# Optimization experiments

Hardware: AMD Instinct MI355X
Metric: run time of the kernel (lower is better)

The kernel has to match this reference:

```python
import jax, jax.numpy as jnp
import numpy as np

# uniform-size batching: B graphs, NC compound atoms, NP pocket residues each
B, NC, NP, H = 16, 64, 384, 128
CFEAT, PFEAT = 56, 1280
SCALE = 5.0  # coordinate_scale
LN_EPS = 1e-5


def setup_inputs() -> dict:
    key = jax.random.key(0)
    ks = jax.random.split(key, 16)
    inp = {
        "compound_feats": jax.random.normal(ks[0], (B * NC, CFEAT), jnp.float32),
        "pocket_feats": jax.random.normal(ks[1], (B * NP, PFEAT), jnp.float32),
        "complex_coords": jax.random.normal(ks[2], (B, 2 + NC + NP, 3), jnp.float32) * 10.0,
        "pocket_xyz": jax.random.normal(ks[3], (B, NP, 3), jnp.float32) * 10.0,
        "dis_map": jax.random.uniform(ks[4], (B * NP * NC,), jnp.float32) * 10.0,
        # learned parameters (xavier with gain=0.001 as in the torch init)
        "Wc": jax.random.normal(ks[5], (CFEAT, H), jnp.float32) * 0.001,
        "bc": jnp.zeros((H,), jnp.float32),
        "Wp": jax.random.normal(ks[6], (PFEAT, H), jnp.float32) * 0.001,
        "bp": jnp.zeros((H,), jnp.float32),
        "ln_g": jnp.ones((H,), jnp.float32),
        "ln_b": jnp.zeros((H,), jnp.float32),
        "W1": jax.random.normal(ks[7], (H, H), jnp.float32) * 0.001,
        "b1": jnp.zeros((H,), jnp.float32),
        "W2": jax.random.normal(ks[8], (H, 1), jnp.float32) * 0.001,
        "b2": jnp.zeros((1,), jnp.float32),
    }
    return inp


def _layernorm(x, g, b):
    m = jnp.mean(x, axis=-1, keepdims=True)
    v = jnp.mean(jnp.square(x - m), axis=-1, keepdims=True)
    return (x - m) * jax.lax.rsqrt(v + LN_EPS) * g + b


def reference(compound_feats, pocket_feats, complex_coords, pocket_xyz, dis_map,
              Wc, bc, Wp, bp, ln_g, ln_b, W1, b1, W2, b2):
    norm = lambda x: x / SCALE
    # input linears, then dense-batch (uniform sizes -> exact reshape)
    comp_emb = (compound_feats @ Wc + bc).reshape(B, NC, H)   # [B,NC,H]
    pock_emb = (pocket_feats @ Wp + bp).reshape(B, NP, H)     # [B,NP,H]
    # complex layout per graph: [glb_c, compound (NC), glb_p, pocket (NP)]
    # complex_binding_model treated as identity (see notes): emb/coords pass through.
    comp_coords_out = norm(complex_coords[:, 1:1 + NC])       # [B,NC,3] (normalized)
    pock_coords = norm(pocket_xyz)                            # [B,NP,3]
    # torch.cdist(pocket, compound): [B,NP,NC]
    diff = pock_coords[:, :, None, :] - comp_coords_out[:, None, :, :]
    pc_dis = jnp.sqrt(jnp.sum(jnp.square(diff), axis=-1))
    # layernorm + pairwise outer product + distmap MLP
    p_ln = _layernorm(pock_emb, ln_g, ln_b)
    c_ln = _layernorm(comp_emb, ln_g, ln_b)
    z = jnp.einsum('bik,bjk->bijk', p_ln, c_ln)               # [B,NP,NC,H]
    h = jax.nn.relu(z @ W1 + b1)
    b_logit = (h @ W2 + b2)[..., 0]                            # [B,NP,NC]
    # uniform sizes -> all-true masks, boolean-select is a flatten
    dis_map_pred_by_pair = jax.nn.sigmoid(b_logit.reshape(-1)) * 10.0
    dis_map_pred_by_coord = jnp.clip(pc_dis.reshape(-1) * SCALE, 0.0, 10.0)
    compound_coord_pred = (comp_coords_out * SCALE).reshape(B * NC, 3)
    compound_batch = jnp.repeat(jnp.arange(B, dtype=jnp.int32), NC)
    return (compound_coord_pred, compound_batch, dis_map_pred_by_pair,
            dis_map_pred_by_coord, dis_map)
```

## Files before the change

### kernel.cpp

```cpp
#include <hip/hip_runtime.h>
#include <hip/hip_bf16.h>

#define BB 16
#define NC 64
#define NP 384
#define HH 128
#define CF 56
#define PFT 1280

typedef float f32x4 __attribute__((ext_vector_type(4)));
typedef __bf16 bf16x8 __attribute__((ext_vector_type(8)));
typedef unsigned short u16x8 __attribute__((ext_vector_type(8)));
typedef unsigned short u16x4 __attribute__((ext_vector_type(4)));

static __device__ __forceinline__ unsigned short f2bfu(float f){
  __bf16 h = (__bf16)f;
  return __builtin_bit_cast(unsigned short, h);
}
static __device__ __forceinline__ float bfu2f(unsigned short u){
  __bf16 h = __builtin_bit_cast(__bf16, u);
  return (float)h;
}

__global__ __launch_bounds__(256) void k_prep(
    const float* __restrict__ cf, const float* __restrict__ Wc,
    const float* __restrict__ bc, const float* __restrict__ lng,
    const float* __restrict__ lnb, const float* __restrict__ Wp,
    const float* __restrict__ W1, const float* __restrict__ cc,
    const float* __restrict__ px, const float* __restrict__ dm,
    unsigned short* __restrict__ c_ln, unsigned short* __restrict__ wpt,
    unsigned short* __restrict__ w1t,
    float* __restrict__ out1, float* __restrict__ out4, float* __restrict__ out5){
  __shared__ unsigned short t[128][72];
  __shared__ float redc[2][2], redc2[2][2];
  int bx = blockIdx.x;
  int tid = threadIdx.x;
  if (bx < 20){
    int k0 = bx*64;
    #pragma unroll
    for (int i=0;i<8;i++){
      int fi = tid + i*256;
      int k  = fi>>5;
      int c4 = (fi&31)*4;
      float4 v = *(const float4*)(Wp + (size_t)(k0+k)*HH + c4);
      t[c4+0][k]=f2bfu(v.x); t[c4+1][k]=f2bfu(v.y);
      t[c4+2][k]=f2bfu(v.z); t[c4+3][k]=f2bfu(v.w);
    }
    __syncthreads();
    #pragma unroll
    for (int i=0;i<4;i++){
      int ci = tid + i*256;
      int col = ci>>3, kb = ci&7;
      u16x8 v = *(const u16x8*)&t[col][kb*8];
      *(u16x8*)(wpt + (size_t)col*PFT + k0 + kb*8) = v;
    }
  } else if (bx < 84){
    int idx = (bx-20)*256+tid;
    int k = idx>>7, m = idx&127;
    w1t[m*HH+k] = f2bfu(W1[idx]);
  } else if (bx < 596){
    int rh = tid>>7, m = tid&127;
    int row = (bx-84)*2 + rh;
    const float* cr = cf + row*CF;
    float acc = bc[m];
    #pragma unroll
    for (int k=0;k<CF;k++) acc += cr[k]*Wc[k*HH+m];
    float s=acc, s2=acc*acc;
    #pragma unroll
    for (int off=1; off<64; off<<=1){ s += __shfl_xor(s,off,64); s2 += __shfl_xor(s2,off,64); }
    int wid = (tid>>6)&1;
    if ((m&63)==0){ redc[rh][wid]=s; redc2[rh][wid]=s2; }
    __syncthreads();
    float S=redc[rh][0]+redc[rh][1], S2=redc2[rh][0]+redc2[rh][1];
    float mean = S*(1.0f/HH);
    float var  = S2*(1.0f/HH) - mean*mean;
    float rs = rsqrtf(var + 1e-5f);
    c_ln[(size_t)row*HH+m] = f2bfu((acc-mean)*rs*lng[m] + lnb[m]);
  } else if (bx < 608){
    int idx = (bx-596)*256+tid;
    if (idx < BB*NC*3){
      int bb = idx/(NC*3), rem = idx%(NC*3);
      float v = cc[(size_t)bb*(2+NC+NP)*3 + 3 + rem];
      out1[idx] = (v/5.0f)*5.0f;
    }
    if (idx < BB*NC) out1[BB*NC*3+idx] = (float)(idx>>6);
  } else {
    int idx = (bx-608)*256+tid;
    int b = idx/(NP*NC), r = idx%(NP*NC), i = r>>6, j = r&63;
    const float* pp = px + ((size_t)b*NP+i)*3;
    const float* cp = cc + (size_t)b*(2+NC+NP)*3 + 3 + (size_t)j*3;
    float dx=pp[0]/5.0f-cp[0]/5.0f;
    float dy=pp[1]/5.0f-cp[1]/5.0f;
    float dz=pp[2]/5.0f-cp[2]/5.0f;
    float d = sqrtf(dx*dx+dy*dy+dz*dz)*5.0f;
    d = fminf(fmaxf(d,0.f),10.f);
    out4[idx]=d;
    out5[idx]=dm[idx];
  }
}

__global__ __launch_bounds__(256,2) void k_main(
    const float* __restrict__ pf, const unsigned short* __restrict__ wpt,
    const float* __restrict__ bp, const float* __restrict__ lng,
    const float* __restrict__ lnb,
    const unsigned short* __restrict__ c_ln, const unsigned short* __restrict__ w1t,
    const float* __restrict__ b1, const float* __restrict__ W2,
    const float* __restrict__ b2p, float* __restrict__ out3){
  __shared__ __align__(16) unsigned short sA[2][16*64];
  __shared__ __align__(16) unsigned short sB[2][HH*64];
  __shared__ __align__(16) float sPf[12*HH];
  int tid = threadIdx.x;
  int w = tid>>6, lane = tid&63, q = lane&15, gr = lane>>4;
  int bx = blockIdx.x;
  int b  = bx>>5;
  int i0 = (bx&31)*12;
  size_t prow0 = (size_t)(b*NP + i0);
  *(unsigned short*)((char*)&sA[0][0] + 1536 + tid*2) = 0;
  *(unsigned short*)((char*)&sA[1][0] + 1536 + tid*2) = 0;
  f32x4 acc2[2];
  acc2[0]=(f32x4){0.f,0.f,0.f,0.f}; acc2[1]=(f32x4){0.f,0.f,0.f,0.f};
  int arow = tid>>4, ak4 = (tid&15)*4;
  float4 ra; u16x8 rb[4];
  #define LOADS1(KS) {                                                         \
    int kbase = (KS)*64;                                                       \
    if (arow < 12)                                                             \
      ra = *(const float4*)(pf + (prow0+arow)*PFT + kbase + ak4);              \
    _Pragma("unroll")                                                          \
    for (int i=0;i<4;i++){                                                     \
      int bi = tid + 256*i;                                                    \
      int col = bi>>3, kb = bi&7;                                              \
      rb[i] = *(const u16x8*)(wpt + (size_t)col*PFT + kbase + kb*8);           \
    }                                                                          \
  }
  #define WRITES1(BUF) {                                                       \
    char* A = (char*)&sA[BUF][0];                                              \
    char* Bc = (char*)&sB[BUF][0];                                             \
    if (arow < 12){                                                            \
      u16x4 h = { f2bfu(ra.x), f2bfu(ra.y), f2bfu(ra.z), f2bfu(ra.w) };        \
      *(u16x4*)(A + arow*128 + (((ak4>>3)^(arow&7))<<4) + ((ak4&7)<<1)) = h;   \
    }                                                                          \
    _Pragma("unroll")                                                          \
    for (int i=0;i<4;i++){                                                     \
      int bi = tid + 256*i;                                                    \
      int col = bi>>3, kb = bi&7;                                              \
      *(u16x8*)(Bc + col*128 + ((kb^(col&7))<<4)) = rb[i];                     \
    }                                                                          \
  }
  LOADS1(0)
  WRITES1(0)
  int cur = 0;
  for (int ks=0; ks<20; ks++){
    if (ks<19) LOADS1(ks+1)
    __syncthreads();
    char* A = (char*)&sA[cur][0];
    char* Bc = (char*)&sB[cur][0];
    #pragma unroll
    for (int kk=0;kk<2;kk++){
      bf16x8 a = *(bf16x8*)(A + q*128 + (((kk*4+gr)^(q&7))<<4));
      #pragma unroll
      for (int ct=0;ct<2;ct++){
        int col = w*32 + ct*16 + q;
        bf16x8 bfr = *(bf16x8*)(Bc + col*128 + (((kk*4+gr)^(col&7))<<4));
        acc2[ct] = __builtin_amdgcn_mfma_f32_16x16x32_bf16(a,bfr,acc2[ct],0,0,0);
      }
    }
    if (ks<19){ WRITES1(cur^1) cur ^= 1; }
  }
  __syncthreads();
  #pragma unroll
  for (int ct=0;ct<2;ct++){
    int col = w*32 + ct*16 + q;
    float bpv = bp[col];
    #pragma unroll
    for (int r=0;r<4;r++){
      int row = gr*4+r;
      if (row < 12) sPf[row*HH + col] = acc2[ct][r] + bpv;
    }
  }
  float cfr[4][8];
  {
    const unsigned short* cb = c_ln + (size_t)b*NC*HH + (size_t)(w*16+q)*HH + gr*8;
    #pragma unroll
    for (int kt=0;kt<4;kt++){
      u16x8 v = *(const u16x8*)(cb + kt*32);
      #pragma unroll
      for (int e=0;e<8;e++) cfr[kt][e] = bfu2f(v[e]);
    }
  }
  bf16x8 w1f[4][8];
  #pragma unroll
  for (int kt=0;kt<4;kt++)
    #pragma unroll
    for (int nt=0;nt<8;nt++)
      w1f[kt][nt] = *(const bf16x8*)(w1t + (size_t)(nt*16+q)*HH + kt*32 + gr*8);
  float b1v[8], w2v[8];
  #pragma unroll
  for (int nt=0;nt<8;nt++){ b1v[nt]=b1[nt*16+q]; w2v[nt]=W2[nt*16+q]; }
  float b2 = b2p[0];
  __syncthreads();
  {
    float g0 = lng[lane], g1 = lng[lane+64];
    float B0 = lnb[lane], B1 = lnb[lane+64];
    #pragma unroll
    for (int rr=0; rr<3; rr++){
      int row = w*3+rr;
      float a0 = sPf[row*HH + lane], a1 = sPf[row*HH + lane + 64];
      float s = a0+a1, s2 = a0*a0 + a1*a1;
      #pragma unroll
      for (int off=1; off<64; off<<=1){ s += __shfl_xor(s,off,64); s2 += __shfl_xor(s2,off,64); }
      float mean = s*(1.0f/HH);
      float var  = s2*(1.0f/HH) - mean*mean;
      float rs   = rsqrtf(var + 1e-5f);
      sPf[row*HH + lane]      = (a0-mean)*rs*g0 + B0;
      sPf[row*HH + lane + 64] = (a1-mean)*rs*g1 + B1;
    }
  }
  __syncthreads();
  for (int ii=0; ii<12; ii++){
    f32x4 acc[8];
    #pragma unroll
    for (int nt=0;nt<8;nt++) acc[nt]=(f32x4){0.f,0.f,0.f,0.f};
    #pragma unroll
    for (int kt=0;kt<4;kt++){
      f32x4 p0 = *(const f32x4*)&sPf[ii*HH + kt*32 + gr*8];
      f32x4 p1 = *(const f32x4*)&sPf[ii*HH + kt*32 + gr*8 + 4];
      bf16x8 a;
      #pragma unroll
      for (int e=0;e<4;e++) a[e]   = (__bf16)(cfr[kt][e]*p0[e]);
      #pragma unroll
      for (int e=0;e<4;e++) a[e+4] = (__bf16)(cfr[kt][e+4]*p1[e]);
      #pragma unroll
      for (int nt=0;nt<8;nt++)
        acc[nt] = __builtin_amdgcn_mfma_f32_16x16x32_bf16(a, w1f[kt][nt], acc[nt], 0,0,0);
    }
    float part[4]={0.f,0.f,0.f,0.f};
    #pragma unroll
    for (int nt=0;nt<8;nt++)
      #pragma unroll
      for (int r=0;r<4;r++){
        float h = acc[nt][r] + b1v[nt];
        h = fmaxf(h, 0.f);
        part[r] += h*w2v[nt];
      }
    #pragma unroll
    for (int r=0;r<4;r++){
      part[r]+=__shfl_xor(part[r],1,16);
      part[r]+=__shfl_xor(part[r],2,16);
      part[r]+=__shfl_xor(part[r],4,16);
      part[r]+=__shfl_xor(part[r],8,16);
    }
    if (q==0){
      float4 o;
      o.x = 10.f/(1.f+expf(-(part[0]+b2)));
      o.y = 10.f/(1.f+expf(-(part[1]+b2)));
      o.z = 10.f/(1.f+expf(-(part[2]+b2)));
      o.w = 10.f/(1.f+expf(-(part[3]+b2)));
      *(float4*)(out3 + (prow0+ii)*NC + w*16 + gr*4) = o;
    }
  }
}

extern "C" void kernel_launch(void* const* d_in, const int* in_sizes, int n_in,
                              void* d_out, int out_size, void* d_ws, size_t ws_size,
                              hipStream_t stream){
  const float* cf = (const float*)d_in[0];
  const float* pf = (const float*)d_in[1];
  const float* cc = (const float*)d_in[2];
  const float* px = (const float*)d_in[3];
  const float* dm = (const float*)d_in[4];
  const float* Wc = (const float*)d_in[5];
  const float* bc = (const float*)d_in[6];
  const float* Wp = (const float*)d_in[7];
  const float* bp = (const float*)d_in[8];
  const float* lng= (const float*)d_in[9];
  const float* lnb= (const float*)d_in[10];
  const float* W1 = (const float*)d_in[11];
  const float* b1 = (const float*)d_in[12];
  const float* W2 = (const float*)d_in[13];
  const float* b2 = (const float*)d_in[14];

  float* out = (float*)d_out;
  char* ws = (char*)d_ws;
  unsigned short* c_ln = (unsigned short*)ws;
  unsigned short* w1t  = (unsigned short*)(ws + 262144 + 1572864);
  unsigned short* wpt  = (unsigned short*)(ws + 262144 + 1572864 + 32768);

  float* out1 = out;
  float* out3 = out + BB*NC*3 + BB*NC;
  float* out4 = out3 + BB*NP*NC;
  float* out5 = out4 + BB*NP*NC;

  hipLaunchKernelGGL(k_prep, dim3(2144), dim3(256), 0, stream,
                     cf, Wc, bc, lng, lnb, Wp, W1, cc, px, dm,
                     c_ln, wpt, w1t, out1, out4, out5);
  hipLaunchKernelGGL(k_main, dim3(512), dim3(256), 0, stream,
                     pf, wpt, bp, lng, lnb, c_ln, w1t, b1, W2, b2, out3);
}
```

Measured before the change: 44.67 us.

## Load pocket GEMM operands directly to registers and use 32x32 MFMA for pair MLP

The pocket projection GEMM drops its LDS double-buffered staging. Each wave now loads A (fp32, converted to bf16) and B fragments straight from global memory into registers, with no barriers in the K loop. The pair MLP switches from 16x16x32 to 32x32x16 MFMA with a 2x2 wave split over compound atoms and hidden units. It processes two pocket rows per iteration and streams W1 fragments from global/L2, and partial logits are combined through shared memory before the sigmoid. This cuts LDS traffic and syncs and raises MFMA efficiency, at the cost of more uncoalesced global loads, a 32-wide shuffle reduction, and dropping the 2-blocks-per-SIMD occupancy hint.

```diff
diff --git a/kernel.cpp b/kernel.cpp
--- a/kernel.cpp
+++ b/kernel.cpp
@@ -9,9 +9,9 @@
 #define PFT 1280
 
 typedef float f32x4 __attribute__((ext_vector_type(4)));
+typedef float f32x16 __attribute__((ext_vector_type(16)));
 typedef __bf16 bf16x8 __attribute__((ext_vector_type(8)));
 typedef unsigned short u16x8 __attribute__((ext_vector_type(8)));
-typedef unsigned short u16x4 __attribute__((ext_vector_type(4)));
 
 static __device__ __forceinline__ unsigned short f2bfu(float f){
   __bf16 h = (__bf16)f;
@@ -99,103 +99,65 @@
   }
 }
 
-__global__ __launch_bounds__(256,2) void k_main(
+__global__ __launch_bounds__(256) void k_main(
     const float* __restrict__ pf, const unsigned short* __restrict__ wpt,
     const float* __restrict__ bp, const float* __restrict__ lng,
     const float* __restrict__ lnb,
     const unsigned short* __restrict__ c_ln, const unsigned short* __restrict__ w1t,
     const float* __restrict__ b1, const float* __restrict__ W2,
     const float* __restrict__ b2p, float* __restrict__ out3){
-  __shared__ __align__(16) unsigned short sA[2][16*64];
-  __shared__ __align__(16) unsigned short sB[2][HH*64];
   __shared__ __align__(16) float sPf[12*HH];
+  __shared__ __align__(16) float psumh[2][12][64];
   int tid = threadIdx.x;
   int w = tid>>6, lane = tid&63, q = lane&15, gr = lane>>4;
   int bx = blockIdx.x;
   int b  = bx>>5;
   int i0 = (bx&31)*12;
   size_t prow0 = (size_t)(b*NP + i0);
-  *(unsigned short*)((char*)&sA[0][0] + 1536 + tid*2) = 0;
-  *(unsigned short*)((char*)&sA[1][0] + 1536 + tid*2) = 0;
   f32x4 acc2[2];
   acc2[0]=(f32x4){0.f,0.f,0.f,0.f}; acc2[1]=(f32x4){0.f,0.f,0.f,0.f};
-  int arow = tid>>4, ak4 = (tid&15)*4;
-  float4 ra; u16x8 rb[4];
-  #define LOADS1(KS) {                                                         \
-    int kbase = (KS)*64;                                                       \
-    if (arow < 12)                                                             \
-      ra = *(const float4*)(pf + (prow0+arow)*PFT + kbase + ak4);              \
-    _Pragma("unroll")                                                          \
-    for (int i=0;i<4;i++){                                                     \
-      int bi = tid + 256*i;                                                    \
-      int col = bi>>3, kb = bi&7;                                              \
-      rb[i] = *(const u16x8*)(wpt + (size_t)col*PFT + kbase + kb*8);           \
-    }                                                                          \
-  }
-  #define WRITES1(BUF) {                                                       \
-    char* A = (char*)&sA[BUF][0];                                              \
-    char* Bc = (char*)&sB[BUF][0];                                             \
-    if (arow < 12){                                                            \
-      u16x4 h = { f2bfu(ra.x), f2bfu(ra.y), f2bfu(ra.z), f2bfu(ra.w) };        \
-      *(u16x4*)(A + arow*128 + (((ak4>>3)^(arow&7))<<4) + ((ak4&7)<<1)) = h;   \
-    }                                                                          \
-    _Pragma("unroll")                                                          \
-    for (int i=0;i<4;i++){                                                     \
-      int bi = tid + 256*i;                                                    \
-      int col = bi>>3, kb = bi&7;                                              \
-      *(u16x8*)(Bc + col*128 + ((kb^(col&7))<<4)) = rb[i];                     \
-    }                                                                          \
-  }
-  LOADS1(0)
-  WRITES1(0)
-  int cur = 0;
+  int arow = q<12 ? q : 11;
+  const float* pA = pf + (prow0+arow)*PFT;
+  const unsigned short* pB0 = wpt + (size_t)(w*32+q)*PFT;
+  const unsigned short* pB1 = wpt + (size_t)(w*32+16+q)*PFT;
+  #pragma unroll 4
   for (int ks=0; ks<20; ks++){
-    if (ks<19) LOADS1(ks+1)
-    __syncthreads();
-    char* A = (char*)&sA[cur][0];
-    char* Bc = (char*)&sB[cur][0];
-    #pragma unroll
-    for (int kk=0;kk<2;kk++){
-      bf16x8 a = *(bf16x8*)(A + q*128 + (((kk*4+gr)^(q&7))<<4));
-      #pragma unroll
-      for (int ct=0;ct<2;ct++){
-        int col = w*32 + ct*16 + q;
-        bf16x8 bfr = *(bf16x8*)(Bc + col*128 + (((kk*4+gr)^(col&7))<<4));
-        acc2[ct] = __builtin_amdgcn_mfma_f32_16x16x32_bf16(a,bfr,acc2[ct],0,0,0);
-      }
-    }
-    if (ks<19){ WRITES1(cur^1) cur ^= 1; }
-  }
-  __syncthreads();
-  #pragma unroll
-  for (int ct=0;ct<2;ct++){
-    int col = w*32 + ct*16 + q;
-    float bpv = bp[col];
+    #pragma unroll
+    for (int kk=0; kk<2; kk++){
+      int k0 = ks*64 + kk*32 + gr*8;
+      float4 a0 = *(const float4*)(pA + k0);
+      float4 a1 = *(const float4*)(pA + k0 + 4);
+      u16x8 ub0 = *(const u16x8*)(pB0 + k0);
+      u16x8 ub1 = *(const u16x8*)(pB1 + k0);
+      bf16x8 a;
+      a[0]=(__bf16)a0.x; a[1]=(__bf16)a0.y; a[2]=(__bf16)a0.z; a[3]=(__bf16)a0.w;
+      a[4]=(__bf16)a1.x; a[5]=(__bf16)a1.y; a[6]=(__bf16)a1.z; a[7]=(__bf16)a1.w;
+      acc2[0] = __builtin_amdgcn_mfma_f32_16x16x32_bf16(a, __builtin_bit_cast(bf16x8, ub0), acc2[0], 0,0,0);
+      acc2[1] = __builtin_amdgcn_mfma_f32_16x16x32_bf16(a, __builtin_bit_cast(bf16x8, ub1), acc2[1], 0,0,0);
+    }
+  }
+  {
+    float bp0 = bp[w*32+q], bp1 = bp[w*32+16+q];
     #pragma unroll
     for (int r=0;r<4;r++){
       int row = gr*4+r;
-      if (row < 12) sPf[row*HH + col] = acc2[ct][r] + bpv;
-    }
-  }
-  float cfr[4][8];
+      if (row<12){
+        sPf[row*HH + w*32+q]      = acc2[0][r] + bp0;
+        sPf[row*HH + w*32+16+q]   = acc2[1][r] + bp1;
+      }
+    }
+  }
+  int l31 = lane&31, gr2 = lane>>5;
+  int jh = w&1, mh = w>>1;
+  int j0 = jh*32, m0 = mh*64;
+  u16x8 cfrag[8];
   {
-    const unsigned short* cb = c_ln + (size_t)b*NC*HH + (size_t)(w*16+q)*HH + gr*8;
-    #pragma unroll
-    for (int kt=0;kt<4;kt++){
-      u16x8 v = *(const u16x8*)(cb + kt*32);
-      #pragma unroll
-      for (int e=0;e<8;e++) cfr[kt][e] = bfu2f(v[e]);
-    }
-  }
-  bf16x8 w1f[4][8];
-  #pragma unroll
-  for (int kt=0;kt<4;kt++)
-    #pragma unroll
-    for (int nt=0;nt<8;nt++)
-      w1f[kt][nt] = *(const bf16x8*)(w1t + (size_t)(nt*16+q)*HH + kt*32 + gr*8);
-  float b1v[8], w2v[8];
-  #pragma unroll
-  for (int nt=0;nt<8;nt++){ b1v[nt]=b1[nt*16+q]; w2v[nt]=W2[nt*16+q]; }
+    const unsigned short* cbase = c_ln + ((size_t)b*NC + j0 + l31)*HH + gr2*8;
+    #pragma unroll
+    for (int ksp=0;ksp<8;ksp++) cfrag[ksp] = *(const u16x8*)(cbase + ksp*16);
+  }
+  float b1v0=b1[m0+l31], b1v1=b1[m0+32+l31];
+  float w2v0=W2[m0+l31], w2v1=W2[m0+32+l31];
   float b2 = b2p[0];
   __syncthreads();
   {
@@ -216,47 +178,71 @@
     }
   }
   __syncthreads();
-  for (int ii=0; ii<12; ii++){
-    f32x4 acc[8];
-    #pragma unroll
-    for (int nt=0;nt<8;nt++) acc[nt]=(f32x4){0.f,0.f,0.f,0.f};
-    #pragma unroll
-    for (int kt=0;kt<4;kt++){
-      f32x4 p0 = *(const f32x4*)&sPf[ii*HH + kt*32 + gr*8];
-      f32x4 p1 = *(const f32x4*)&sPf[ii*HH + kt*32 + gr*8 + 4];
-      bf16x8 a;
-      #pragma unroll
-      for (int e=0;e<4;e++) a[e]   = (__bf16)(cfr[kt][e]*p0[e]);
-      #pragma unroll
-      for (int e=0;e<4;e++) a[e+4] = (__bf16)(cfr[kt][e+4]*p1[e]);
-      #pragma unroll
-      for (int nt=0;nt<8;nt++)
-        acc[nt] = __builtin_amdgcn_mfma_f32_16x16x32_bf16(a, w1f[kt][nt], acc[nt], 0,0,0);
-    }
-    float part[4]={0.f,0.f,0.f,0.f};
-    #pragma unroll
-    for (int nt=0;nt<8;nt++)
-      #pragma unroll
-      for (int r=0;r<4;r++){
-        float h = acc[nt][r] + b1v[nt];
-        h = fmaxf(h, 0.f);
-        part[r] += h*w2v[nt];
+  const unsigned short* wb0 = w1t + (size_t)(m0+l31)*HH + gr2*8;
+  const unsigned short* wb1 = w1t + (size_t)(m0+32+l31)*HH + gr2*8;
+  for (int ip=0; ip<6; ip++){
+    f32x16 accA0, accA1, accB0, accB1;
+    #pragma unroll
+    for (int r=0;r<16;r++){ accA0[r]=0.f; accA1[r]=0.f; accB0[r]=0.f; accB1[r]=0.f; }
+    int iiA = ip*2, iiB = ip*2+1;
+    #pragma unroll
+    for (int ksp=0; ksp<8; ksp++){
+      bf16x8 bv0 = __builtin_bit_cast(bf16x8, *(const u16x8*)(wb0 + ksp*16));
+      bf16x8 bv1 = __builtin_bit_cast(bf16x8, *(const u16x8*)(wb1 + ksp*16));
+      u16x8 cfv = cfrag[ksp];
+      {
+        f32x4 p0 = *(const f32x4*)&sPf[iiA*HH + ksp*16 + gr2*8];
+        f32x4 p1 = *(const f32x4*)&sPf[iiA*HH + ksp*16 + gr2*8 + 4];
+        bf16x8 a;
+        a[0]=(__bf16)(bfu2f(cfv[0])*p0[0]); a[1]=(__bf16)(bfu2f(cfv[1])*p0[1]);
+        a[2]=(__bf16)(bfu2f(cfv[2])*p0[2]); a[3]=(__bf16)(bfu2f(cfv[3])*p0[3]);
+        a[4]=(__bf16)(bfu2f(cfv[4])*p1[0]); a[5]=(__bf16)(bfu2f(cfv[5])*p1[1]);
+        a[6]=(__bf16)(bfu2f(cfv[6])*p1[2]); a[7]=(__bf16)(bfu2f(cfv[7])*p1[3]);
+        accA0 = __builtin_amdgcn_mfma_f32_32x32x16_bf16(a, bv0, accA0, 0,0,0);
+        accA1 = __builtin_amdgcn_mfma_f32_32x32x16_bf16(a, bv1, accA1, 0,0,0);
       }
-    #pragma unroll
-    for (int r=0;r<4;r++){
-      part[r]+=__shfl_xor(part[r],1,16);
-      part[r]+=__shfl_xor(part[r],2,16);
-      part[r]+=__shfl_xor(part[r],4,16);
-      part[r]+=__shfl_xor(part[r],8,16);
-    }
-    if (q==0){
-      float4 o;
-      o.x = 10.f/(1.f+expf(-(part[0]+b2)));
-      o.y = 10.f/(1.f+expf(-(part[1]+b2)));
-      o.z = 10.f/(1.f+expf(-(part[2]+b2)));
-      o.w = 10.f/(1.f+expf(-(part[3]+b2)));
-      *(float4*)(out3 + (prow0+ii)*NC + w*16 + gr*4) = o;
-    }
+      {
+        f32x4 p0 = *(const f32x4*)&sPf[iiB*HH + ksp*16 + gr2*8];
+        f32x4 p1 = *(const f32x4*)&sPf[iiB*HH + ksp*16 + gr2*8 + 4];
+        bf16x8 a;
+        a[0]=(__bf16)(bfu2f(cfv[0])*p0[0]); a[1]=(__bf16)(bfu2f(cfv[1])*p0[1]);
+        a[2]=(__bf16)(bfu2f(cfv[2])*p0[2]); a[3]=(__bf16)(bfu2f(cfv[3])*p0[3]);
+        a[4]=(__bf16)(bfu2f(cfv[4])*p1[0]); a[5]=(__bf16)(bfu2f(cfv[5])*p1[1]);
+        a[6]=(__bf16)(bfu2f(cfv[6])*p1[2]); a[7]=(__bf16)(bfu2f(cfv[7])*p1[3]);
+        accB0 = __builtin_amdgcn_mfma_f32_32x32x16_bf16(a, bv0, accB0, 0,0,0);
+        accB1 = __builtin_amdgcn_mfma_f32_32x32x16_bf16(a, bv1, accB1, 0,0,0);
+      }
+    }
+    #define EPILOG(A0, A1, III) {                                              \
+      float part[16];                                                          \
+      _Pragma("unroll")                                                        \
+      for (int r=0;r<16;r++){                                                  \
+        float h0 = fmaxf(A0[r]+b1v0, 0.f);                                     \
+        float h1 = fmaxf(A1[r]+b1v1, 0.f);                                     \
+        part[r] = h0*w2v0 + h1*w2v1;                                           \
+      }                                                                        \
+      _Pragma("unroll")                                                        \
+      for (int off=1; off<32; off<<=1){                                        \
+        _Pragma("unroll")                                                      \
+        for (int r=0;r<16;r++) part[r] += __shfl_xor(part[r], off, 64);        \
+      }                                                                        \
+      if (l31==0){                                                             \
+        _Pragma("unroll")                                                      \
+        for (int r=0;r<16;r++){                                                \
+          int row = (r&3) + 8*(r>>2) + 4*gr2;                                  \
+          psumh[mh][III][j0+row] = part[r];                                    \
+        }                                                                      \
+      }                                                                        \
+    }
+    EPILOG(accA0, accA1, iiA)
+    EPILOG(accB0, accB1, iiB)
+    #undef EPILOG
+  }
+  __syncthreads();
+  for (int v=tid; v<12*64; v+=256){
+    int ii = v>>6, j = v&63;
+    float s = psumh[0][ii][j] + psumh[1][ii][j] + b2;
+    out3[(prow0+ii)*NC + j] = 10.f/(1.f+expf(-s));
   }
 }
 
```

New measurement: 88.25 us. 1.98x slower.
